# Kernel optimization log

Measured on AMD Instinct MI355X. Metric: run time of the kernel, lower is better.

## Reference

```python
import jax, jax.numpy as jnp
import numpy as np

N = 100000      # nodes
E = 1600000     # edges
G = 128         # graphs in batch
D_IN = 20       # node_feat_dim
D_EMB = 300     # emb_dim
D_OUT = 64      # output_feats
L_REST = 4      # layers 1..4 (num_layers=5 total)
BN_EPS = 1e-5


def setup_inputs() -> dict:
    key = jax.random.key(0)
    ks = jax.random.split(key, 24)
    s = 0.05
    node_feats = jax.random.normal(ks[0], (N, D_IN), jnp.float32)
    edge_feats = jax.random.normal(ks[1], (E, 1), jnp.float32)
    src = jax.random.randint(ks[2], (E,), 0, N, dtype=jnp.int32)
    dst = jax.random.randint(ks[3], (E,), 0, N, dtype=jnp.int32)
    graph_ids = jnp.sort(jax.random.randint(ks[4], (N,), 0, G, dtype=jnp.int32))
    # layer 0: D_IN -> 2*D_EMB -> D_EMB, BN(D_EMB)
    w1_0 = jax.random.normal(ks[5], (D_IN, 2 * D_EMB), jnp.float32) * s
    b1_0 = jnp.zeros((2 * D_EMB,), jnp.float32)
    w2_0 = jax.random.normal(ks[6], (2 * D_EMB, D_EMB), jnp.float32) * s
    b2_0 = jnp.zeros((D_EMB,), jnp.float32)
    gamma_0 = jnp.ones((D_EMB,), jnp.float32)
    beta_0 = jnp.zeros((D_EMB,), jnp.float32)
    # layers 1..4: D_EMB -> 2*D_EMB -> D_EMB, BN(D_EMB), stacked
    w1 = jax.random.normal(ks[7], (L_REST, D_EMB, 2 * D_EMB), jnp.float32) * s
    b1 = jnp.zeros((L_REST, 2 * D_EMB), jnp.float32)
    w2 = jax.random.normal(ks[8], (L_REST, 2 * D_EMB, D_EMB), jnp.float32) * s
    b2 = jnp.zeros((L_REST, D_EMB), jnp.float32)
    gamma = jnp.ones((L_REST, D_EMB), jnp.float32)
    beta = jnp.zeros((L_REST, D_EMB), jnp.float32)
    # final transform Linear(300, 64)
    wt = jax.random.normal(ks[9], (D_EMB, D_OUT), jnp.float32) * s
    bt = jnp.zeros((D_OUT,), jnp.float32)
    return {"node_feats": node_feats, "edge_feats": edge_feats, "src": src,
            "dst": dst, "graph_ids": graph_ids,
            "w1_0": w1_0, "b1_0": b1_0, "w2_0": w2_0, "b2_0": b2_0,
            "gamma_0": gamma_0, "beta_0": beta_0,
            "w1": w1, "b1": b1, "w2": w2, "b2": b2,
            "gamma": gamma, "beta": beta, "wt": wt, "bt": bt}


def _gin_layer(x, e, src, dst, w1, b1, w2, b2, g, b):
    # u_add_e: gather source node feats, add (broadcast) edge feats -> [E, d]
    m = x[src] + e
    # sum aggregation to destination nodes -> [N, d]
    agg = jax.ops.segment_sum(m, dst, num_segments=N)
    # MLP: Linear -> ReLU -> Linear
    h = jnp.maximum(agg @ w1 + b1, 0.0) @ w2 + b2
    # BatchNorm1d with batch statistics (biased var), affine
    mu = h.mean(axis=0)
    var = h.var(axis=0)
    h = (h - mu) * jax.lax.rsqrt(var + BN_EPS) * g + b
    return h  # no activation (GINLayer activation=None); dropout is eval-mode identity


def reference(node_feats, edge_feats, src, dst, graph_ids,
              w1_0, b1_0, w2_0, b2_0, gamma_0, beta_0,
              w1, b1, w2, b2, gamma, beta, wt, bt):
    h = _gin_layer(node_feats, edge_feats, src, dst,
                   w1_0, b1_0, w2_0, b2_0, gamma_0, beta_0)
    for l in range(L_REST):
        h = _gin_layer(h, edge_feats, src, dst,
                       w1[l], b1[l], w2[l], b2[l], gamma[l], beta[l])
    # AvgPooling readout per graph
    sums = jax.ops.segment_sum(h, graph_ids, num_segments=G)          # [G, D_EMB]
    counts = jax.ops.segment_sum(jnp.ones((N,), h.dtype), graph_ids, num_segments=G)
    graph_feats = sums / jnp.maximum(counts, 1.0)[:, None]
    return graph_feats @ wt + bt  # [G, D_OUT]
```

## Files before the change

### kernel.cpp

```cpp
#include <hip/hip_runtime.h>

#define NN 100000
#define NE 1600000
#define NG 128
#define DIN 20
#define DEMB 300
#define DHID 600
#define DOUT 64
#define DIN_P 32
#define EMB_P 320
#define HID_P 640
#define SCAN_BLK 392
#define KSTG 320

static const float BN_EPS_F = 1e-5f;

typedef _Float16 f16x8 __attribute__((ext_vector_type(8)));
typedef float f32x4 __attribute__((ext_vector_type(4)));

__device__ __forceinline__ void gload_lds16(const void* g, const void* l) {
  __builtin_amdgcn_global_load_lds(
      (const __attribute__((address_space(1))) unsigned int*)(unsigned long long)g,
      (__attribute__((address_space(3))) unsigned int*)(unsigned long long)(unsigned int)(unsigned long long)l,
      16, 0, 0);
}


__global__ void count_edges_kernel(const int* __restrict__ dst, const float* __restrict__ ef,
                                   int* __restrict__ counts, float* __restrict__ esum) {
  int e = blockIdx.x * blockDim.x + threadIdx.x;
  if (e >= NE) return;
  int v = dst[e];
  atomicAdd(&counts[v], 1);
  atomicAdd(&esum[v], ef[e]);
}

__global__ __launch_bounds__(256) void scan_part1(const int* __restrict__ counts,
                                                  int* __restrict__ bsums) {
  __shared__ int red[256];
  int t = threadIdx.x;
  int i = blockIdx.x * 256 + t;
  red[t] = (i < NN) ? counts[i] : 0;
  __syncthreads();
  for (int s = 128; s > 0; s >>= 1) {
    if (t < s) red[t] += red[t + s];
    __syncthreads();
  }
  if (t == 0) bsums[blockIdx.x] = red[0];
}

__global__ __launch_bounds__(512) void scan_part2(const int* __restrict__ bsums,
                                                  int* __restrict__ boffs) {
  __shared__ int sc[512];
  int t = threadIdx.x;
  int v = (t < SCAN_BLK) ? bsums[t] : 0;
  sc[t] = v;
  __syncthreads();
  for (int off = 1; off < 512; off <<= 1) {
    int u = (t >= off) ? sc[t - off] : 0;
    __syncthreads();
    sc[t] += u;
    __syncthreads();
  }
  if (t < SCAN_BLK) boffs[t] = sc[t] - v;
}

__global__ __launch_bounds__(256) void scan_part3(const int* __restrict__ counts,
                                                  const int* __restrict__ boffs,
                                                  int* __restrict__ row_ptr,
                                                  int* __restrict__ cursor) {
  __shared__ int sc[256];
  int t = threadIdx.x;
  int i = blockIdx.x * 256 + t;
  int v = (i < NN) ? counts[i] : 0;
  sc[t] = v;
  __syncthreads();
  for (int off = 1; off < 256; off <<= 1) {
    int u = (t >= off) ? sc[t - off] : 0;
    __syncthreads();
    sc[t] += u;
    __syncthreads();
  }
  if (i < NN) {
    int excl = sc[t] - v + boffs[blockIdx.x];
    row_ptr[i] = excl;
    cursor[i] = excl;
  }
  if (i == NN - 1) row_ptr[NN] = NE;
}

__global__ void scatter_kernel(const int* __restrict__ src, const int* __restrict__ dst,
                               int* __restrict__ cursor, int* __restrict__ csr_src) {
  int e = blockIdx.x * blockDim.x + threadIdx.x;
  if (e >= NE) return;
  int pos = atomicAdd(&cursor[dst[e]], 1);
  csr_src[pos] = src[e];
}


__global__ void repack_wt_kernel(const float* __restrict__ w, _Float16* __restrict__ out,
                                 int K, int Nsrc, int Np, int Kp) {
  int idx = blockIdx.x * blockDim.x + threadIdx.x;
  if (idx >= Np * Kp) return;
  int n = idx / Kp, k = idx - n * Kp;
  float v = (n < Nsrc && k < K) ? w[(size_t)k * Nsrc + n] : 0.f;
  out[idx] = (_Float16)v;
}

__global__ void pad_bias_kernel(const float* __restrict__ b, float* __restrict__ out, int n, int np) {
  int i = blockIdx.x * blockDim.x + threadIdx.x;
  if (i >= np) return;
  out[i] = (i < n) ? b[i] : 0.f;
}


__global__ __launch_bounds__(256) void spmm0_kernel(const float* __restrict__ x,
                                                    const int* __restrict__ row_ptr,
                                                    const int* __restrict__ csr_src,
                                                    const float* __restrict__ esum,
                                                    _Float16* __restrict__ out) {
  int wid = (blockIdx.x * blockDim.x + threadIdx.x) >> 6;
  int lane = threadIdx.x & 63;
  if (wid >= NN) return;
  int beg = row_ptr[wid], end = row_ptr[wid + 1];
  float acc = 0.f;
  int j = beg;
  for (; j + 1 < end; j += 2) {
    int s0 = csr_src[j], s1 = csr_src[j + 1];
    if (lane < DIN) {
      acc += x[(size_t)s0 * DIN + lane];
      acc += x[(size_t)s1 * DIN + lane];
    }
  }
  if (j < end) {
    int s0 = csr_src[j];
    if (lane < DIN) acc += x[(size_t)s0 * DIN + lane];
  }
  if (lane < DIN_P) {
    float v = (lane < DIN) ? acc + esum[wid] : 0.f;
    out[(size_t)wid * DIN_P + lane] = (_Float16)v;
  }
}


__global__ __launch_bounds__(256) void spmm_f16_kernel(const _Float16* __restrict__ x,
                                                       const float* __restrict__ scale,
                                                       const float* __restrict__ shift,
                                                       const int* __restrict__ row_ptr,
                                                       const int* __restrict__ csr_src,
                                                       const float* __restrict__ esum,
                                                       _Float16* __restrict__ out) {
  int wid = (blockIdx.x * blockDim.x + threadIdx.x) >> 6;
  int lane = threadIdx.x & 63;
  if (wid >= NN) return;
  int beg = row_ptr[wid], end = row_ptr[wid + 1];
  float deg = (float)(end - beg);
  float es = esum[wid];
  if (lane >= 40) return;
  const f16x8* xb = (const f16x8*)x;
  float acc[8] = {};
  int j = beg;
  for (; j + 7 < end; j += 8) {
    int s0 = csr_src[j + 0], s1 = csr_src[j + 1], s2 = csr_src[j + 2], s3 = csr_src[j + 3];
    int s4 = csr_src[j + 4], s5 = csr_src[j + 5], s6 = csr_src[j + 6], s7 = csr_src[j + 7];
    f16x8 v0 = xb[(size_t)s0 * 40 + lane];
    f16x8 v1 = xb[(size_t)s1 * 40 + lane];
    f16x8 v2 = xb[(size_t)s2 * 40 + lane];
    f16x8 v3 = xb[(size_t)s3 * 40 + lane];
    f16x8 v4 = xb[(size_t)s4 * 40 + lane];
    f16x8 v5 = xb[(size_t)s5 * 40 + lane];
    f16x8 v6 = xb[(size_t)s6 * 40 + lane];
    f16x8 v7 = xb[(size_t)s7 * 40 + lane];
#pragma unroll
    for (int i = 0; i < 8; ++i) {
      acc[i] += ((float)v0[i] + (float)v1[i]) + ((float)v2[i] + (float)v3[i]) +
                ((float)v4[i] + (float)v5[i]) + ((float)v6[i] + (float)v7[i]);
    }
  }
  for (; j < end; ++j) {
    f16x8 v0 = xb[(size_t)csr_src[j] * 40 + lane];
#pragma unroll
    for (int i = 0; i < 8; ++i) acc[i] += (float)v0[i];
  }
  int c = lane * 8;
  f16x8 o;
#pragma unroll
  for (int i = 0; i < 8; ++i)
    o[i] = (_Float16)(acc[i] * scale[c + i] + deg * shift[c + i] + es);
  ((f16x8*)(out))[(size_t)wid * 40 + lane] = o;
}


template <bool RELU, bool STATS>
__global__ __launch_bounds__(256, 4) void gemm_blds_kernel(const _Float16* __restrict__ A,
                                                           const _Float16* __restrict__ Bt,
                                                           const float* __restrict__ bias,
                                                           _Float16* __restrict__ C,
                                                           int M, int K, int ldC,
                                                           float* __restrict__ stats) {
  __shared__ __align__(16) _Float16 lds[64 * KSTG];
  const int t = threadIdx.x;
  const int wv = t >> 6;
  const int lane = t & 63;
  const int fm = lane & 15;
  const int k8 = (lane >> 4) * 8;
  const int m0 = blockIdx.y * 128;
  const int n0 = blockIdx.x * 64;

  const _Float16* Ap[2];
#pragma unroll
  for (int rg = 0; rg < 2; ++rg) {
    int r = min(m0 + wv * 32 + rg * 16 + fm, M - 1);
    Ap[rg] = A + (size_t)r * K + k8;
  }

  f32x4 acc[2][4] = {};
  const int nkc_tot = K >> 5;

  for (int ks0 = 0; ks0 < K; ks0 += KSTG) {
    const int klen = min(KSTG, K - ks0);
    const int nkc = klen >> 5;
    const int NCH = nkc << 2;
    for (int c = wv; c < NCH; c += 4) {
      int kc = c >> 2, ni = c & 3;
      gload_lds16(Bt + (size_t)(n0 + ni * 16 + fm) * K + ks0 + kc * 32 + k8,
                  &lds[c * 512 + lane * 8]);
    }
    __syncthreads();

    f16x8 a[2];
    a[0] = *(const f16x8*)(Ap[0] + ks0);
    a[1] = *(const f16x8*)(Ap[1] + ks0);
    for (int kc = 0; kc < nkc; ++kc) {
      f16x8 an[2];
      int knext = ks0 + (kc + 1) * 32;
      if (knext < K) {
        an[0] = *(const f16x8*)(Ap[0] + knext);
        an[1] = *(const f16x8*)(Ap[1] + knext);
      }
      f16x8 b[4];
#pragma unroll
      for (int ni = 0; ni < 4; ++ni) b[ni] = *(const f16x8*)&lds[(kc * 4 + ni) * 512 + lane * 8];
#pragma unroll
      for (int rg = 0; rg < 2; ++rg)
#pragma unroll
        for (int ni = 0; ni < 4; ++ni)
          acc[rg][ni] = __builtin_amdgcn_mfma_f32_16x16x32_f16(a[rg], b[ni], acc[rg][ni], 0, 0, 0);
      if (knext < K) { a[0] = an[0]; a[1] = an[1]; }
    }
    if (ks0 + KSTG < K) __syncthreads();
  }
  (void)nkc_tot;

  float bi[4];
#pragma unroll
  for (int ni = 0; ni < 4; ++ni) bi[ni] = bias[n0 + ni * 16 + fm];
  const int rq = (lane >> 4) * 4;
  float ssum[4] = {}, ssq[4] = {};
#pragma unroll
  for (int rg = 0; rg < 2; ++rg) {
#pragma unroll
    for (int ni = 0; ni < 4; ++ni) {
      int col = n0 + ni * 16 + fm;
#pragma unroll
      for (int r = 0; r < 4; ++r) {
        int row = m0 + wv * 32 + rg * 16 + rq + r;
        float v = acc[rg][ni][r] + bi[ni];
        if (RELU) v = fmaxf(v, 0.f);
        if (row < M) {
          C[(size_t)row * ldC + col] = (_Float16)v;
          if (STATS) { ssum[ni] += v; ssq[ni] += v * v; }
        }
      }
    }
  }
  if (STATS) {
    __syncthreads();
    float* sred = (float*)lds;
    if (t < 128) sred[t] = 0.f;
    __syncthreads();
#pragma unroll
    for (int ni = 0; ni < 4; ++ni) {
      atomicAdd(&sred[ni * 16 + fm], ssum[ni]);
      atomicAdd(&sred[64 + ni * 16 + fm], ssq[ni]);
    }
    __syncthreads();
    if (t < 64) {
      atomicAdd(&stats[n0 + t], sred[t]);
      atomicAdd(&stats[EMB_P + n0 + t], sred[64 + t]);
    }
  }
}


__global__ void bn_finalize_kernel(const float* __restrict__ stats, const float* __restrict__ gamma,
                                   const float* __restrict__ beta, float* __restrict__ scale,
                                   float* __restrict__ shift) {
  int c = threadIdx.x;
  if (c >= EMB_P) return;
  if (c < DEMB) {
    float mu = stats[c] / (float)NN;
    float var = fmaxf(stats[EMB_P + c] / (float)NN - mu * mu, 0.f);
    float sc = gamma[c] * rsqrtf(var + BN_EPS_F);
    scale[c] = sc;
    shift[c] = beta[c] - mu * sc;
  } else {
    scale[c] = 0.f;
    shift[c] = 0.f;
  }
}


#define POOL_BLOCKS 784

__global__ __launch_bounds__(256) void pool2_kernel(const _Float16* __restrict__ h,
                                                    const int* __restrict__ gid,
                                                    float* __restrict__ graw) {
  const int w = (blockIdx.x * 256 + threadIdx.x) >> 6;
  const int lane = threadIdx.x & 63;
  const int NW = POOL_BLOCKS * 4;
  const int rpw = (NN + NW - 1) / NW;
  int r0 = w * rpw, r1 = min(r0 + rpw, NN);
  if (r0 >= r1 || lane >= 40) return;
  const f16x8* hb = (const f16x8*)h;
  float acc[8] = {};
  int curg = gid[r0];
  for (int r = r0; r < r1; ++r) {
    int g = gid[r];
    if (g != curg) {
#pragma unroll
      for (int i = 0; i < 8; ++i) {
        atomicAdd(&graw[curg * EMB_P + lane * 8 + i], acc[i]);
        acc[i] = 0.f;
      }
      curg = g;
    }
    f16x8 v = hb[(size_t)r * 40 + lane];
#pragma unroll
    for (int i = 0; i < 8; ++i) acc[i] += (float)v[i];
  }
#pragma unroll
  for (int i = 0; i < 8; ++i) atomicAdd(&graw[curg * EMB_P + lane * 8 + i], acc[i]);
}

__global__ void final_kernel(const float* __restrict__ graw, const int* __restrict__ gid,
                             const float* __restrict__ scale, const float* __restrict__ shift,
                             const float* __restrict__ wt, const float* __restrict__ bt,
                             float* __restrict__ out) {
  int g = blockIdx.x, t = threadIdx.x;
  __shared__ int sb[2];
  if (t < 2) {
    int target = g + t;
    int lo = 0, hi = NN;
    while (lo < hi) {
      int m = (lo + hi) >> 1;
      if (gid[m] < target) lo = m + 1; else hi = m;
    }
    sb[t] = lo;
  }
  __syncthreads();
  int cnt = sb[1] - sb[0];
  float inv = cnt > 0 ? 1.0f / (float)cnt : 0.f;
  float sh_on = cnt > 0 ? 1.0f : 0.f;
  float acc = bt[t];
  const float* row = graw + g * EMB_P;
  for (int k = 0; k < DEMB; ++k) {
    float gf = row[k] * inv * scale[k] + sh_on * shift[k];
    acc = fmaf(gf, wt[k * DOUT + t], acc);
  }
  out[g * DOUT + t] = acc;
}


extern "C" void kernel_launch(void* const* d_in, const int* in_sizes, int n_in,
                              void* d_out, int out_size, void* d_ws, size_t ws_size,
                              hipStream_t stream) {
  const float* node_feats = (const float*)d_in[0];
  const float* edge_feats = (const float*)d_in[1];
  const int* src = (const int*)d_in[2];
  const int* dst = (const int*)d_in[3];
  const int* gid = (const int*)d_in[4];
  const float* w1_0 = (const float*)d_in[5];
  const float* b1_0 = (const float*)d_in[6];
  const float* w2_0 = (const float*)d_in[7];
  const float* b2_0 = (const float*)d_in[8];
  const float* gamma_0 = (const float*)d_in[9];
  const float* beta_0 = (const float*)d_in[10];
  const float* w1s = (const float*)d_in[11];
  const float* b1s = (const float*)d_in[12];
  const float* w2s = (const float*)d_in[13];
  const float* b2s = (const float*)d_in[14];
  const float* gammas = (const float*)d_in[15];
  const float* betas = (const float*)d_in[16];
  const float* wt = (const float*)d_in[17];
  const float* bt = (const float*)d_in[18];
  float* out = (float*)d_out;
  (void)in_sizes; (void)n_in; (void)out_size; (void)ws_size;

  char* ws = (char*)d_ws;
  size_t off = 0;
  auto carve = [&](size_t bytes) -> void* {
    void* p = ws + off;
    off += (bytes + 255) & ~(size_t)255;
    return p;
  };
  _Float16* P0 = (_Float16*)carve((size_t)NN * EMB_P * 2);
  _Float16* P1 = (_Float16*)carve((size_t)NN * EMB_P * 2);
  _Float16* Q  = (_Float16*)carve((size_t)NN * HID_P * 2);
  float* esum   = (float*)carve((size_t)NN * 4);
  int* counts   = (int*)carve((size_t)NN * 4);
  int* row_ptr  = (int*)carve((size_t)(NN + 1) * 4);
  int* cursor   = (int*)carve((size_t)NN * 4);
  int* csr_src  = (int*)carve((size_t)NE * 4);
  int* bsums    = (int*)carve((size_t)SCAN_BLK * 4);
  int* boffs    = (int*)carve((size_t)SCAN_BLK * 4);
  _Float16* w1t0 = (_Float16*)carve((size_t)HID_P * DIN_P * 2);
  _Float16* w1t  = (_Float16*)carve((size_t)4 * HID_P * EMB_P * 2);
  _Float16* w2t  = (_Float16*)carve((size_t)5 * EMB_P * HID_P * 2);
  float* b1p   = (float*)carve((size_t)5 * HID_P * 4);
  float* b2p   = (float*)carve((size_t)5 * EMB_P * 4);
  float* stats = (float*)carve(2 * EMB_P * 4);
  float* scale = (float*)carve(EMB_P * 4);
  float* shift = (float*)carve(EMB_P * 4);
  float* graw  = (float*)carve((size_t)NG * EMB_P * 4);

  hipMemsetAsync(esum, 0, (size_t)NN * 4, stream);
  hipMemsetAsync(counts, 0, (size_t)NN * 4, stream);
  hipMemsetAsync(graw, 0, (size_t)NG * EMB_P * 4, stream);

  count_edges_kernel<<<(NE + 255) / 256, 256, 0, stream>>>(dst, edge_feats, counts, esum);
  scan_part1<<<SCAN_BLK, 256, 0, stream>>>(counts, bsums);
  scan_part2<<<1, 512, 0, stream>>>(bsums, boffs);
  scan_part3<<<SCAN_BLK, 256, 0, stream>>>(counts, boffs, row_ptr, cursor);
  scatter_kernel<<<(NE + 255) / 256, 256, 0, stream>>>(src, dst, cursor, csr_src);

  repack_wt_kernel<<<(HID_P * DIN_P + 255) / 256, 256, 0, stream>>>(w1_0, w1t0, DIN, DHID, HID_P, DIN_P);
  for (int l = 0; l < 4; ++l) {
    repack_wt_kernel<<<(HID_P * EMB_P + 255) / 256, 256, 0, stream>>>(
        w1s + (size_t)l * DEMB * DHID, w1t + (size_t)l * HID_P * EMB_P, DEMB, DHID, HID_P, EMB_P);
  }
  repack_wt_kernel<<<(EMB_P * HID_P + 255) / 256, 256, 0, stream>>>(w2_0, w2t, DHID, DEMB, EMB_P, HID_P);
  for (int l = 0; l < 4; ++l) {
    repack_wt_kernel<<<(EMB_P * HID_P + 255) / 256, 256, 0, stream>>>(
        w2s + (size_t)l * DHID * DEMB, w2t + (size_t)(l + 1) * EMB_P * HID_P, DHID, DEMB, EMB_P, HID_P);
  }
  pad_bias_kernel<<<(HID_P + 255) / 256, 256, 0, stream>>>(b1_0, b1p, DHID, HID_P);
  pad_bias_kernel<<<(EMB_P + 255) / 256, 256, 0, stream>>>(b2_0, b2p, DEMB, EMB_P);
  for (int l = 0; l < 4; ++l) {
    pad_bias_kernel<<<(HID_P + 255) / 256, 256, 0, stream>>>(b1s + (size_t)l * DHID, b1p + (size_t)(l + 1) * HID_P, DHID, HID_P);
    pad_bias_kernel<<<(EMB_P + 255) / 256, 256, 0, stream>>>(b2s + (size_t)l * DEMB, b2p + (size_t)(l + 1) * EMB_P, DEMB, EMB_P);
  }

  const int MT = (NN + 127) / 128;
  const int spmm_blocks = (NN * 64 + 255) / 256;

  for (int l = 0; l < 5; ++l) {
    const _Float16* w1t_l = (l == 0) ? w1t0 : w1t + (size_t)(l - 1) * HID_P * EMB_P;
    const _Float16* w2t_l = w2t + (size_t)l * EMB_P * HID_P;
    const float* b1p_l = b1p + (size_t)l * HID_P;
    const float* b2p_l = b2p + (size_t)l * EMB_P;
    const float* ga = (l == 0) ? gamma_0 : gammas + (size_t)(l - 1) * DEMB;
    const float* be = (l == 0) ? beta_0 : betas + (size_t)(l - 1) * DEMB;
    int K1 = (l == 0) ? DIN_P : EMB_P;

    if (l == 0) {
      spmm0_kernel<<<spmm_blocks, 256, 0, stream>>>(node_feats, row_ptr, csr_src, esum, P0);
    } else {
      spmm_f16_kernel<<<spmm_blocks, 256, 0, stream>>>(P1, scale, shift, row_ptr, csr_src, esum, P0);
    }

    gemm_blds_kernel<true, false><<<dim3(HID_P / 64, MT), 256, 0, stream>>>(
        P0, w1t_l, b1p_l, Q, NN, K1, HID_P, nullptr);

    hipMemsetAsync(stats, 0, 2 * EMB_P * 4, stream);
    gemm_blds_kernel<false, true><<<dim3(EMB_P / 64, MT), 256, 0, stream>>>(
        Q, w2t_l, b2p_l, P1, NN, HID_P, EMB_P, stats);

    bn_finalize_kernel<<<1, EMB_P, 0, stream>>>(stats, ga, be, scale, shift);
  }

  pool2_kernel<<<POOL_BLOCKS, 256, 0, stream>>>(P1, gid, graw);
  final_kernel<<<NG, 64, 0, stream>>>(graw, gid, scale, shift, wt, bt, out);
}
```

Measured before the change: 2.577 ms.

## Retile GEMM to 64x320 blocks with double-buffered per-K-chunk weight staging

The MFMA GEMM changes from 128x64 output tiles, which staged up to 320 K-columns of weights into LDS at once, to 64x320 tiles. Each wave now computes a 32x160 sub-tile, and the weights stream through a two-buffer LDS ring one 32-wide K chunk at a time, with the next chunk prefetched while the current one is computed. The aim is to read each A row far fewer times across N-blocks and to overlap weight loads with MFMA work. The trade-offs are 20 accumulators per wave, which raises register pressure (launch bounds drop to 3), a barrier every K chunk, and fewer blocks when M is small. BN stats reduction is widened to cover the 320 columns per block.

```diff
diff --git a/kernel.cpp b/kernel.cpp
--- a/kernel.cpp
+++ b/kernel.cpp
@@ -11,7 +11,6 @@
 #define EMB_P 320
 #define HID_P 640
 #define SCAN_BLK 392
-#define KSTG 320
 
 static const float BN_EPS_F = 1e-5f;
 
@@ -192,80 +191,74 @@
 
 
 template <bool RELU, bool STATS>
-__global__ __launch_bounds__(256, 4) void gemm_blds_kernel(const _Float16* __restrict__ A,
-                                                           const _Float16* __restrict__ Bt,
-                                                           const float* __restrict__ bias,
-                                                           _Float16* __restrict__ C,
-                                                           int M, int K, int ldC,
-                                                           float* __restrict__ stats) {
-  __shared__ __align__(16) _Float16 lds[64 * KSTG];
+__global__ __launch_bounds__(256, 3) void gemm_nb_kernel(const _Float16* __restrict__ A,
+                                                         const _Float16* __restrict__ Bt,
+                                                         const float* __restrict__ bias,
+                                                         _Float16* __restrict__ C,
+                                                         int M, int K, int ldC,
+                                                         float* __restrict__ stats) {
+  __shared__ __align__(16) _Float16 lds[2][20 * 512];
   const int t = threadIdx.x;
   const int wv = t >> 6;
   const int lane = t & 63;
   const int fm = lane & 15;
   const int k8 = (lane >> 4) * 8;
-  const int m0 = blockIdx.y * 128;
-  const int n0 = blockIdx.x * 64;
+  const int m0 = blockIdx.y * 64;
+  const int n0 = blockIdx.x * 320;
+  const int wm = (wv >> 1) * 32;
+  const int wnf = (wv & 1) * 10;
 
   const _Float16* Ap[2];
 #pragma unroll
   for (int rg = 0; rg < 2; ++rg) {
-    int r = min(m0 + wv * 32 + rg * 16 + fm, M - 1);
+    int r = min(m0 + wm + rg * 16 + fm, M - 1);
     Ap[rg] = A + (size_t)r * K + k8;
   }
 
-  f32x4 acc[2][4] = {};
-  const int nkc_tot = K >> 5;
-
-  for (int ks0 = 0; ks0 < K; ks0 += KSTG) {
-    const int klen = min(KSTG, K - ks0);
-    const int nkc = klen >> 5;
-    const int NCH = nkc << 2;
-    for (int c = wv; c < NCH; c += 4) {
-      int kc = c >> 2, ni = c & 3;
-      gload_lds16(Bt + (size_t)(n0 + ni * 16 + fm) * K + ks0 + kc * 32 + k8,
-                  &lds[c * 512 + lane * 8]);
-    }
-    __syncthreads();
-
-    f16x8 a[2];
-    a[0] = *(const f16x8*)(Ap[0] + ks0);
-    a[1] = *(const f16x8*)(Ap[1] + ks0);
-    for (int kc = 0; kc < nkc; ++kc) {
-      f16x8 an[2];
-      int knext = ks0 + (kc + 1) * 32;
-      if (knext < K) {
-        an[0] = *(const f16x8*)(Ap[0] + knext);
-        an[1] = *(const f16x8*)(Ap[1] + knext);
-      }
-      f16x8 b[4];
-#pragma unroll
-      for (int ni = 0; ni < 4; ++ni) b[ni] = *(const f16x8*)&lds[(kc * 4 + ni) * 512 + lane * 8];
-#pragma unroll
-      for (int rg = 0; rg < 2; ++rg)
-#pragma unroll
-        for (int ni = 0; ni < 4; ++ni)
-          acc[rg][ni] = __builtin_amdgcn_mfma_f32_16x16x32_f16(a[rg], b[ni], acc[rg][ni], 0, 0, 0);
-      if (knext < K) { a[0] = an[0]; a[1] = an[1]; }
-    }
-    if (ks0 + KSTG < K) __syncthreads();
-  }
-  (void)nkc_tot;
-
-  float bi[4];
-#pragma unroll
-  for (int ni = 0; ni < 4; ++ni) bi[ni] = bias[n0 + ni * 16 + fm];
+  const int nkc = K >> 5;
+  for (int c = wv; c < 20; c += 4)
+    gload_lds16(Bt + (size_t)(n0 + c * 16 + fm) * K + k8, &lds[0][c * 512 + lane * 8]);
+
+  f32x4 acc[2][10] = {};
+  f16x8 a0 = *(const f16x8*)Ap[0];
+  f16x8 a1 = *(const f16x8*)Ap[1];
+
+  for (int kc = 0; kc < nkc; ++kc) {
+    __syncthreads();
+    if (kc + 1 < nkc) {
+      for (int c = wv; c < 20; c += 4)
+        gload_lds16(Bt + (size_t)(n0 + c * 16 + fm) * K + (kc + 1) * 32 + k8,
+                    &lds[(kc + 1) & 1][c * 512 + lane * 8]);
+    }
+    f16x8 an0, an1;
+    if (kc + 1 < nkc) {
+      an0 = *(const f16x8*)(Ap[0] + (kc + 1) * 32);
+      an1 = *(const f16x8*)(Ap[1] + (kc + 1) * 32);
+    }
+    const _Float16* bb = lds[kc & 1];
+#pragma unroll
+    for (int ni = 0; ni < 10; ++ni) {
+      f16x8 b = *(const f16x8*)&bb[(wnf + ni) * 512 + lane * 8];
+      acc[0][ni] = __builtin_amdgcn_mfma_f32_16x16x32_f16(a0, b, acc[0][ni], 0, 0, 0);
+      acc[1][ni] = __builtin_amdgcn_mfma_f32_16x16x32_f16(a1, b, acc[1][ni], 0, 0, 0);
+    }
+    if (kc + 1 < nkc) { a0 = an0; a1 = an1; }
+  }
+
   const int rq = (lane >> 4) * 4;
-  float ssum[4] = {}, ssq[4] = {};
+  float ssum[10], ssq[10];
+#pragma unroll
+  for (int ni = 0; ni < 10; ++ni) { ssum[ni] = 0.f; ssq[ni] = 0.f; }
 #pragma unroll
   for (int rg = 0; rg < 2; ++rg) {
 #pragma unroll
-    for (int ni = 0; ni < 4; ++ni) {
-      int col = n0 + ni * 16 + fm;
+    for (int ni = 0; ni < 10; ++ni) {
+      int col = n0 + (wnf + ni) * 16 + fm;
+      float bi = bias[col];
 #pragma unroll
       for (int r = 0; r < 4; ++r) {
-        int row = m0 + wv * 32 + rg * 16 + rq + r;
-        float v = acc[rg][ni][r] + bi[ni];
+        int row = m0 + wm + rg * 16 + rq + r;
+        float v = acc[rg][ni][r] + bi;
         if (RELU) v = fmaxf(v, 0.f);
         if (row < M) {
           C[(size_t)row * ldC + col] = (_Float16)v;
@@ -277,17 +270,18 @@
   if (STATS) {
     __syncthreads();
     float* sred = (float*)lds;
-    if (t < 128) sred[t] = 0.f;
-    __syncthreads();
-#pragma unroll
-    for (int ni = 0; ni < 4; ++ni) {
-      atomicAdd(&sred[ni * 16 + fm], ssum[ni]);
-      atomicAdd(&sred[64 + ni * 16 + fm], ssq[ni]);
-    }
-    __syncthreads();
-    if (t < 64) {
-      atomicAdd(&stats[n0 + t], sred[t]);
-      atomicAdd(&stats[EMB_P + n0 + t], sred[64 + t]);
+    for (int i = t; i < 640; i += 256) sred[i] = 0.f;
+    __syncthreads();
+#pragma unroll
+    for (int ni = 0; ni < 10; ++ni) {
+      int c = (wnf + ni) * 16 + fm;
+      atomicAdd(&sred[c], ssum[ni]);
+      atomicAdd(&sred[320 + c], ssq[ni]);
+    }
+    __syncthreads();
+    for (int c = t; c < 320; c += 256) {
+      atomicAdd(&stats[n0 + c], sred[c]);
+      atomicAdd(&stats[EMB_P + n0 + c], sred[320 + c]);
     }
   }
 }
@@ -451,7 +445,7 @@
     pad_bias_kernel<<<(EMB_P + 255) / 256, 256, 0, stream>>>(b2s + (size_t)l * DEMB, b2p + (size_t)(l + 1) * EMB_P, DEMB, EMB_P);
   }
 
-  const int MT = (NN + 127) / 128;
+  const int MB = (NN + 63) / 64;
   const int spmm_blocks = (NN * 64 + 255) / 256;
 
   for (int l = 0; l < 5; ++l) {
@@ -469,11 +463,11 @@
       spmm_f16_kernel<<<spmm_blocks, 256, 0, stream>>>(P1, scale, shift, row_ptr, csr_src, esum, P0);
     }
 
-    gemm_blds_kernel<true, false><<<dim3(HID_P / 64, MT), 256, 0, stream>>>(
+    gemm_nb_kernel<true, false><<<dim3(HID_P / 320, MB), 256, 0, stream>>>(
         P0, w1t_l, b1p_l, Q, NN, K1, HID_P, nullptr);
 
     hipMemsetAsync(stats, 0, 2 * EMB_P * 4, stream);
-    gemm_blds_kernel<false, true><<<dim3(EMB_P / 64, MT), 256, 0, stream>>>(
+    gemm_nb_kernel<false, true><<<dim3(EMB_P / 320, MB), 256, 0, stream>>>(
         Q, w2t_l, b2p_l, P1, NN, HID_P, EMB_P, stats);
 
     bn_finalize_kernel<<<1, EMB_P, 0, stream>>>(stats, ga, be, scale, shift);
```

Measured after the change: 2.692 ms. 4.5% more time.
